# Kernel optimization log

Hardware: AMD Instinct MI355X
Metric: run time of the kernel (lower is better)

## Reference

```python
import jax, jax.numpy as jnp
import numpy as np

B, H, I = 4096, 256, 32


def setup_inputs() -> dict:
    key = jax.random.key(0)
    k1, k2, k3, k4, k5 = jax.random.split(key, 5)
    idx = jax.random.randint(k1, (B,), 0, I)
    inp = jax.nn.one_hot(idx, I, dtype=jnp.float32)  # one-hot selector [B, I]
    hx = jax.random.normal(k2, (B, H), jnp.float32)
    weight_hh = jax.random.normal(k3, (3 * H, H, I), jnp.float32)
    bias_ih = jax.random.normal(k4, (3 * H, I), jnp.float32)
    bias_hh = jax.random.normal(k5, (3 * H, I), jnp.float32)
    return {"input": inp, "hx": hx, "weight_hh": weight_hh,
            "bias_ih": bias_ih, "bias_hh": bias_hh}


def reference(input, hx, weight_hh, bias_ih, bias_hh):
    # input is one-hot, so the broadcast-multiply-sum over the last axis is
    # mathematically a gather of the selected expert slice.
    idx = jnp.argmax(input, axis=-1)                      # [B]
    Wt = jnp.moveaxis(weight_hh, 2, 0)[idx]               # [B, 3H, H] selected recurrent weights
    rec = jnp.einsum('bgh,bh->bg', Wt, hx)                # [B, 3H]
    gates_i = bias_ih.T[idx]                              # [B, 3H]
    gates_h = rec + bias_hh.T[idx]                        # [B, 3H]
    ri, ui, ni = jnp.split(gates_i, 3, axis=1)
    rh, uh, nh = jnp.split(gates_h, 3, axis=1)
    reset_gate = jax.nn.sigmoid(ri + rh)
    update_gate = jax.nn.sigmoid(ui + uh)
    new_gate = jnp.tanh(ni + reset_gate * nh)
    hy = update_gate * hx + (1 - update_gate) * new_gate  # [B, H]
    return hy[None]
```

## Files before the change

kernel.cpp:

```cpp
#include <hip/hip_runtime.h>
#include <math.h>

#define B_N 4096
#define H_N 256
#define I_N 32
#define G3  768

#define NSLOT_AFF 192
#define NSLOT_TOT 336
#define BKT_CAP   24

#define WS_IDX     0
#define WS_SLOTS   16640
#define WS_SORTED  20480
#define WS_B4      36864
#define WS_W5      167936
#define WS_NEEDED  12750848

typedef __attribute__((ext_vector_type(8))) _Float16 f16x8_t;
typedef __attribute__((ext_vector_type(4))) float f32x4_t;

__device__ __forceinline__ float sigm(float x) { return 1.0f / (1.0f + expf(-x)); }

__global__ __launch_bounds__(256) void k_aux(
    const float* __restrict__ w, unsigned short* __restrict__ w5,
    const float* __restrict__ b_ih, const float* __restrict__ b_hh,
    float4* __restrict__ b4,
    const float* __restrict__ inp, int* __restrict__ idx_arr)
{
    int bid = blockIdx.x;
    int t = threadIdx.x;
    if (bid < 768) {
        __shared__ float tl[8 * 1057];
        int r0 = (bid >> 3) * 8;
        int ks = bid & 7;
#pragma unroll
        for (int it = 0; it < 8; ++it) {
            int f4 = it * 256 + t;
            int e4 = (f4 & 7) * 4, hh = (f4 >> 3) & 31, r = f4 >> 8;
            float4 v = *(const float4*)(w + ((size_t)(r0 + r) * 256 + ks * 32 + hh) * 32 + e4);
            int bse = r * 1057 + hh * 33 + e4;
            tl[bse] = v.x; tl[bse + 1] = v.y; tl[bse + 2] = v.z; tl[bse + 3] = v.w;
        }
        __syncthreads();
        int rowgrp = r0 >> 4;
        int mbase = r0 & 15;
#pragma unroll
        for (int it = 0; it < 4; ++it) {
            int c = it * 256 + t;
            int m8 = c & 7, kg = (c >> 3) & 3, e = c >> 5;
            union { _Float16 h[8]; uint4 v; } hi;
#pragma unroll
            for (int t8 = 0; t8 < 8; ++t8) {
                float f = tl[m8 * 1057 + (kg * 8 + t8) * 33 + e];
                hi.h[t8] = (_Float16)f;
            }
            size_t chunk = ((size_t)(e * 8 + ks) * 48 + rowgrp) * 64 + kg * 16 + mbase + m8;
            ((uint4*)w5)[chunk] = hi.v;
        }
    } else if (bid < 800) {
        int bb = bid - 768;
        int e = t & 31;
        int tt = bb * 8 + (t >> 5);
        float r = b_ih[tt * 32 + e] + b_hh[tt * 32 + e];
        float u = b_ih[(256 + tt) * 32 + e] + b_hh[(256 + tt) * 32 + e];
        float ni = b_ih[(512 + tt) * 32 + e];
        float nh = b_hh[(512 + tt) * 32 + e];
        float4 o = {r, u, ni, nh};
        b4[e * 256 + tt] = o;
    } else {
        int b = (bid - 800) * 256 + t;
        const float4* p = (const float4*)(inp + (size_t)b * I_N);
        int idx = 0;
#pragma unroll
        for (int k = 0; k < 8; ++k) {
            float4 v = p[k];
            if (v.x > 0.5f) idx = k * 4 + 0;
            if (v.y > 0.5f) idx = k * 4 + 1;
            if (v.z > 0.5f) idx = k * 4 + 2;
            if (v.w > 0.5f) idx = k * 4 + 3;
        }
        idx_arr[b] = idx;
    }
}

__global__ void k_plan(const int* __restrict__ idx_arr, int* __restrict__ slots,
                       int* __restrict__ sorted) {
    __shared__ int hist[32], offs_l[32], lcur[32];
    __shared__ int bcur[8], ovf;
    int t = threadIdx.x;
    if (t < 32) hist[t] = 0;
    if (t < 8) bcur[t] = 0;
    if (t == 0) ovf = 0;
    __syncthreads();
    for (int i = t; i < B_N; i += 512) atomicAdd(&hist[idx_arr[i]], 1);
    __syncthreads();
    if (t == 0) {
        int run = 0;
        for (int e = 0; e < 32; ++e) { offs_l[e] = run; run += hist[e]; }
    }
    __syncthreads();
    if (t < 32) lcur[t] = offs_l[t];
    for (int s = t; s < NSLOT_TOT; s += 512) slots[s] = -1;
    __syncthreads();
    for (int c = t; c < 32 * 128; c += 512) {
        int e = c >> 7, ch = c & 127;
        int cnt = hist[e];
        if (ch * 32 < cnt) {
            int M = cnt - ch * 32; if (M > 32) M = 32;
            int base = offs_l[e] + ch * 32;
            int item = (e << 18) | (base << 6) | M;
            int bkt = e & 7;
            int j = atomicAdd(&bcur[bkt], 1);
            if (j < BKT_CAP) slots[bkt + 8 * j] = item;
            else { int k = atomicAdd(&ovf, 1); slots[NSLOT_AFF + k] = item; }
        }
    }
    for (int b = t; b < B_N; b += 512) {
        int e = idx_arr[b];
        int pos = atomicAdd(&lcur[e], 1);
        sorted[pos] = b;
    }
}

__global__ __launch_bounds__(256) void k_gemm_mfma(
    const unsigned short* __restrict__ w5,
    const float* __restrict__ hx, const float4* __restrict__ b4,
    const int* __restrict__ sorted, const int* __restrict__ slots,
    float* __restrict__ out)
{
    int item = slots[blockIdx.x];
    if (item < 0) return;
    int e = item >> 18, base = (item >> 6) & 0xfff, M = item & 63;

    __shared__ _Float16 Ah[32 * 256];
    __shared__ int bids[32];

    int t = threadIdx.x;
    {
        int row = t >> 3, c8 = t & 7;
        int b = (row < M) ? sorted[base + row] : -1;
        if (c8 == 0) bids[row] = b;
        if (b >= 0) {
            const float* src = hx + ((size_t)b << 8) + c8 * 32;
            float fv[32];
#pragma unroll
            for (int p = 0; p < 8; ++p)
                *(float4*)&fv[p * 4] = *(const float4*)(src + p * 4);
#pragma unroll
            for (int p = 0; p < 4; ++p) {
                union { _Float16 h[8]; uint4 v; } hu;
#pragma unroll
                for (int jj = 0; jj < 8; ++jj)
                    hu.h[jj] = (_Float16)fv[p * 8 + jj];
                int col = (c8 * 4 + p) ^ (row & 7);
                *(uint4*)&Ah[row * 256 + col * 8] = hu.v;
            }
        } else {
            uint4 z = {0, 0, 0, 0};
#pragma unroll
            for (int p = 0; p < 4; ++p) {
                int col = (c8 * 4 + p) ^ (row & 7);
                *(uint4*)&Ah[row * 256 + col * 8] = z;
            }
        }
    }
    __syncthreads();

    int lane = t & 63, wv = t >> 6;
    int m16 = lane & 15, kg = lane >> 4;
    int q = blockIdx.y * 4 + wv;

    f32x4_t acc[2][3];
#pragma unroll
    for (int tl2 = 0; tl2 < 2; ++tl2)
#pragma unroll
        for (int g = 0; g < 3; ++g) acc[tl2][g] = (f32x4_t){0.f, 0.f, 0.f, 0.f};

    const unsigned short* b_p = w5 + ((size_t)(e * 8) * 48 + q) * 512 + (size_t)lane * 8;

#pragma unroll
    for (int ks = 0; ks < 8; ++ks) {
        int ch = ks * 4 + kg;
        int sw = (ch ^ (m16 & 7)) << 3;
        f16x8_t a_0 = *(const f16x8_t*)&Ah[m16 * 256 + sw];
        f16x8_t a_1 = *(const f16x8_t*)&Ah[(16 + m16) * 256 + sw];
#pragma unroll
        for (int g = 0; g < 3; ++g) {
            size_t foff = ((size_t)ks * 48 + g * 16) * 512;
            f16x8_t b_h = *(const f16x8_t*)(b_p + foff);
            acc[0][g] = __builtin_amdgcn_mfma_f32_16x16x32_f16(a_0, b_h, acc[0][g], 0, 0, 0);
            acc[1][g] = __builtin_amdgcn_mfma_f32_16x16x32_f16(a_1, b_h, acc[1][g], 0, 0, 0);
        }
    }

    int mg = (lane >> 4) * 4;
    int tt = q * 16 + m16;
    float4 bs = b4[e * 256 + tt];
#pragma unroll
    for (int tl2 = 0; tl2 < 2; ++tl2) {
#pragma unroll
        for (int i = 0; i < 4; ++i) {
            int mr = tl2 * 16 + mg + i;
            if (mr < M) {
                int b = bids[mr];
                float x = hx[(size_t)b * 256 + tt];
                float r = sigm(acc[tl2][0][i] + bs.x);
                float u = sigm(acc[tl2][1][i] + bs.y);
                float n = tanhf(bs.z + r * (acc[tl2][2][i] + bs.w));
                out[(size_t)b * 256 + tt] = u * x + (1.0f - u) * n;
            }
        }
    }
}

__global__ void k_naive(const float* __restrict__ inp, const float* __restrict__ hx,
                        const float* __restrict__ w, const float* __restrict__ b_ih,
                        const float* __restrict__ b_hh, float* __restrict__ out) {
    int b = blockIdx.x;
    int t = threadIdx.x;
    __shared__ float sx[H_N];
    __shared__ int sidx;
    if (t == 0) {
        int idx = 0;
        for (int i = 0; i < I_N; ++i)
            if (inp[b * I_N + i] > 0.5f) idx = i;
        sidx = idx;
    }
    sx[t] = hx[b * H_N + t];
    __syncthreads();
    int i = sidx;
    float a0 = 0.f, a1 = 0.f, a2 = 0.f;
    for (int h = 0; h < H_N; ++h) {
        float xv = sx[h];
        a0 = fmaf(w[(t * H_N + h) * I_N + i], xv, a0);
        a1 = fmaf(w[((256 + t) * H_N + h) * I_N + i], xv, a1);
        a2 = fmaf(w[((512 + t) * H_N + h) * I_N + i], xv, a2);
    }
    float r = sigm(b_ih[t * I_N + i] + a0 + b_hh[t * I_N + i]);
    float u = sigm(b_ih[(256 + t) * I_N + i] + a1 + b_hh[(256 + t) * I_N + i]);
    float n = tanhf(b_ih[(512 + t) * I_N + i] + r * (a2 + b_hh[(512 + t) * I_N + i]));
    out[b * H_N + t] = u * sx[t] + (1.0f - u) * n;
}

extern "C" void kernel_launch(void* const* d_in, const int* in_sizes, int n_in,
                              void* d_out, int out_size, void* d_ws, size_t ws_size,
                              hipStream_t stream) {
    const float* inp  = (const float*)d_in[0];
    const float* hx   = (const float*)d_in[1];
    const float* w    = (const float*)d_in[2];
    const float* b_ih = (const float*)d_in[3];
    const float* b_hh = (const float*)d_in[4];
    float* out = (float*)d_out;

    if (ws_size < (size_t)WS_NEEDED) {
        k_naive<<<B_N, H_N, 0, stream>>>(inp, hx, w, b_ih, b_hh, out);
        return;
    }

    char* ws = (char*)d_ws;
    int* idx_arr = (int*)(ws + WS_IDX);
    int* slots   = (int*)(ws + WS_SLOTS);
    int* sorted  = (int*)(ws + WS_SORTED);
    float4* b4   = (float4*)(ws + WS_B4);
    unsigned short* w5 = (unsigned short*)(ws + WS_W5);

    k_aux<<<816, 256, 0, stream>>>(w, w5, b_ih, b_hh, b4, inp, idx_arr);
    k_plan<<<1, 512, 0, stream>>>(idx_arr, slots, sorted);
    k_gemm_mfma<<<dim3(NSLOT_TOT, 4), 256, 0, stream>>>(w5, hx, b4,
                                                        sorted, slots, out);
}
```

Before: 30.26 us.

## Drop single-block planning kernel; bucket rows per segment in aux and plan inside GEMM

Removes the one-block k_plan launch. The index blocks of k_aux now build per-segment expert histograms and local buckets. The GEMM kernel computes per-expert totals and chunk assignments itself and loops over chunks in a grid-stride fashion, finding each row's batch id by prefix-scanning the 16 segment counts. Also switches to __expf-based sigmoid and a fast clamped tanh. This saves one serialized launch and its single-block latency, at the cost of redundant count scans in every GEMM block and slightly lower transcendental accuracy.

```diff
diff --git a/kernel.cpp b/kernel.cpp
--- a/kernel.cpp
+++ b/kernel.cpp
@@ -5,28 +5,31 @@
 #define H_N 256
 #define I_N 32
 #define G3  768
-
-#define NSLOT_AFF 192
-#define NSLOT_TOT 336
-#define BKT_CAP   24
-
-#define WS_IDX     0
-#define WS_SLOTS   16640
-#define WS_SORTED  20480
-#define WS_B4      36864
-#define WS_W5      167936
-#define WS_NEEDED  12750848
+#define NSEG 16
+#define BKROW 4096
+
+#define WS_SC      0
+#define WS_BUCKET  2048
+#define WS_B4      526336
+#define WS_W5      657408
+#define WS_NEEDED  13240320
 
 typedef __attribute__((ext_vector_type(8))) _Float16 f16x8_t;
 typedef __attribute__((ext_vector_type(4))) float f32x4_t;
 
-__device__ __forceinline__ float sigm(float x) { return 1.0f / (1.0f + expf(-x)); }
+__device__ __forceinline__ float sigm(float x) { return 1.0f / (1.0f + __expf(-x)); }
+__device__ __forceinline__ float tanh_fast(float x) {
+    float xc = fminf(fmaxf(x, -15.f), 15.f);
+    float t = __expf(2.f * xc);
+    return (t - 1.f) / (t + 1.f);
+}
 
 __global__ __launch_bounds__(256) void k_aux(
     const float* __restrict__ w, unsigned short* __restrict__ w5,
     const float* __restrict__ b_ih, const float* __restrict__ b_hh,
     float4* __restrict__ b4,
-    const float* __restrict__ inp, int* __restrict__ idx_arr)
+    const float* __restrict__ inp, int* __restrict__ sc,
+    int* __restrict__ bucket)
 {
     int bid = blockIdx.x;
     int t = threadIdx.x;
@@ -69,7 +72,11 @@
         float4 o = {r, u, ni, nh};
         b4[e * 256 + tt] = o;
     } else {
-        int b = (bid - 800) * 256 + t;
+        __shared__ int lhist[32];
+        int seg = bid - 800;
+        if (t < 32) lhist[t] = 0;
+        __syncthreads();
+        int b = seg * 256 + t;
         const float4* p = (const float4*)(inp + (size_t)b * I_N);
         int idx = 0;
 #pragma unroll
@@ -80,67 +87,59 @@
             if (v.z > 0.5f) idx = k * 4 + 2;
             if (v.w > 0.5f) idx = k * 4 + 3;
         }
-        idx_arr[b] = idx;
-    }
-}
-
-__global__ void k_plan(const int* __restrict__ idx_arr, int* __restrict__ slots,
-                       int* __restrict__ sorted) {
-    __shared__ int hist[32], offs_l[32], lcur[32];
-    __shared__ int bcur[8], ovf;
-    int t = threadIdx.x;
-    if (t < 32) hist[t] = 0;
-    if (t < 8) bcur[t] = 0;
-    if (t == 0) ovf = 0;
-    __syncthreads();
-    for (int i = t; i < B_N; i += 512) atomicAdd(&hist[idx_arr[i]], 1);
-    __syncthreads();
-    if (t == 0) {
-        int run = 0;
-        for (int e = 0; e < 32; ++e) { offs_l[e] = run; run += hist[e]; }
-    }
-    __syncthreads();
-    if (t < 32) lcur[t] = offs_l[t];
-    for (int s = t; s < NSLOT_TOT; s += 512) slots[s] = -1;
-    __syncthreads();
-    for (int c = t; c < 32 * 128; c += 512) {
-        int e = c >> 7, ch = c & 127;
-        int cnt = hist[e];
-        if (ch * 32 < cnt) {
-            int M = cnt - ch * 32; if (M > 32) M = 32;
-            int base = offs_l[e] + ch * 32;
-            int item = (e << 18) | (base << 6) | M;
-            int bkt = e & 7;
-            int j = atomicAdd(&bcur[bkt], 1);
-            if (j < BKT_CAP) slots[bkt + 8 * j] = item;
-            else { int k = atomicAdd(&ovf, 1); slots[NSLOT_AFF + k] = item; }
-        }
-    }
-    for (int b = t; b < B_N; b += 512) {
-        int e = idx_arr[b];
-        int pos = atomicAdd(&lcur[e], 1);
-        sorted[pos] = b;
+        int lp = atomicAdd(&lhist[idx], 1);
+        bucket[idx * BKROW + seg * 256 + lp] = b;
+        __syncthreads();
+        if (t < 32) sc[seg * 32 + t] = lhist[t];
     }
 }
 
 __global__ __launch_bounds__(256) void k_gemm_mfma(
     const unsigned short* __restrict__ w5,
     const float* __restrict__ hx, const float4* __restrict__ b4,
-    const int* __restrict__ sorted, const int* __restrict__ slots,
+    const int* __restrict__ sc, const int* __restrict__ bucket,
     float* __restrict__ out)
 {
-    int item = slots[blockIdx.x];
-    if (item < 0) return;
-    int e = item >> 18, base = (item >> 6) & 0xfff, M = item & 63;
+    int bkt = blockIdx.x & 7, j0 = blockIdx.x >> 3;
+    int t = threadIdx.x;
+
+    int tot[4], nch[4];
+#pragma unroll
+    for (int i = 0; i < 4; ++i) {
+        int e = bkt + 8 * i, s = 0;
+#pragma unroll
+        for (int j = 0; j < NSEG; ++j) s += sc[j * 32 + e];
+        tot[i] = s; nch[i] = (s + 31) >> 5;
+    }
+    int c1 = nch[0], c2 = c1 + nch[1], c3 = c2 + nch[2], ntot = c3 + nch[3];
 
     __shared__ _Float16 Ah[32 * 256];
     __shared__ int bids[32];
 
-    int t = threadIdx.x;
-    {
+    for (int jj = j0; jj < ntot; jj += 34) {
+        int ei, ch;
+        if (jj < c1)      { ei = 0; ch = jj; }
+        else if (jj < c2) { ei = 1; ch = jj - c1; }
+        else if (jj < c3) { ei = 2; ch = jj - c2; }
+        else              { ei = 3; ch = jj - c3; }
+        int e = bkt + 8 * ei;
+        int M = tot[ei] - ch * 32; if (M > 32) M = 32;
+
         int row = t >> 3, c8 = t & 7;
-        int b = (row < M) ? sorted[base + row] : -1;
+        int b = -1;
+        if (row < M) {
+            int rank = ch * 32 + row;
+            int acc = 0, seg = 0, off = 0;
+#pragma unroll
+            for (int j = 0; j < NSEG; ++j) {
+                int c = sc[j * 32 + e];
+                if (rank >= acc && rank < acc + c) { seg = j; off = rank - acc; }
+                acc += c;
+            }
+            b = bucket[e * BKROW + seg * 256 + off];
+        }
         if (c8 == 0) bids[row] = b;
+
         if (b >= 0) {
             const float* src = hx + ((size_t)b << 8) + c8 * 32;
             float fv[32];
@@ -151,8 +150,8 @@
             for (int p = 0; p < 4; ++p) {
                 union { _Float16 h[8]; uint4 v; } hu;
 #pragma unroll
-                for (int jj = 0; jj < 8; ++jj)
-                    hu.h[jj] = (_Float16)fv[p * 8 + jj];
+                for (int jj2 = 0; jj2 < 8; ++jj2)
+                    hu.h[jj2] = (_Float16)fv[p * 8 + jj2];
                 int col = (c8 * 4 + p) ^ (row & 7);
                 *(uint4*)&Ah[row * 256 + col * 8] = hu.v;
             }
@@ -164,53 +163,54 @@
                 *(uint4*)&Ah[row * 256 + col * 8] = z;
             }
         }
-    }
-    __syncthreads();
-
-    int lane = t & 63, wv = t >> 6;
-    int m16 = lane & 15, kg = lane >> 4;
-    int q = blockIdx.y * 4 + wv;
-
-    f32x4_t acc[2][3];
-#pragma unroll
-    for (int tl2 = 0; tl2 < 2; ++tl2)
-#pragma unroll
-        for (int g = 0; g < 3; ++g) acc[tl2][g] = (f32x4_t){0.f, 0.f, 0.f, 0.f};
-
-    const unsigned short* b_p = w5 + ((size_t)(e * 8) * 48 + q) * 512 + (size_t)lane * 8;
-
-#pragma unroll
-    for (int ks = 0; ks < 8; ++ks) {
-        int ch = ks * 4 + kg;
-        int sw = (ch ^ (m16 & 7)) << 3;
-        f16x8_t a_0 = *(const f16x8_t*)&Ah[m16 * 256 + sw];
-        f16x8_t a_1 = *(const f16x8_t*)&Ah[(16 + m16) * 256 + sw];
-#pragma unroll
-        for (int g = 0; g < 3; ++g) {
-            size_t foff = ((size_t)ks * 48 + g * 16) * 512;
-            f16x8_t b_h = *(const f16x8_t*)(b_p + foff);
-            acc[0][g] = __builtin_amdgcn_mfma_f32_16x16x32_f16(a_0, b_h, acc[0][g], 0, 0, 0);
-            acc[1][g] = __builtin_amdgcn_mfma_f32_16x16x32_f16(a_1, b_h, acc[1][g], 0, 0, 0);
-        }
-    }
-
-    int mg = (lane >> 4) * 4;
-    int tt = q * 16 + m16;
-    float4 bs = b4[e * 256 + tt];
-#pragma unroll
-    for (int tl2 = 0; tl2 < 2; ++tl2) {
-#pragma unroll
-        for (int i = 0; i < 4; ++i) {
-            int mr = tl2 * 16 + mg + i;
-            if (mr < M) {
-                int b = bids[mr];
-                float x = hx[(size_t)b * 256 + tt];
-                float r = sigm(acc[tl2][0][i] + bs.x);
-                float u = sigm(acc[tl2][1][i] + bs.y);
-                float n = tanhf(bs.z + r * (acc[tl2][2][i] + bs.w));
-                out[(size_t)b * 256 + tt] = u * x + (1.0f - u) * n;
-            }
-        }
+        __syncthreads();
+
+        int lane = t & 63, wv = t >> 6;
+        int m16 = lane & 15, kg = lane >> 4;
+        int q = blockIdx.y * 4 + wv;
+
+        f32x4_t acc2[2][3];
+#pragma unroll
+        for (int tl2 = 0; tl2 < 2; ++tl2)
+#pragma unroll
+            for (int g = 0; g < 3; ++g) acc2[tl2][g] = (f32x4_t){0.f, 0.f, 0.f, 0.f};
+
+        const unsigned short* b_p = w5 + ((size_t)(e * 8) * 48 + q) * 512 + (size_t)lane * 8;
+
+#pragma unroll
+        for (int ks = 0; ks < 8; ++ks) {
+            int chs = ks * 4 + kg;
+            int sw = (chs ^ (m16 & 7)) << 3;
+            f16x8_t a_0 = *(const f16x8_t*)&Ah[m16 * 256 + sw];
+            f16x8_t a_1 = *(const f16x8_t*)&Ah[(16 + m16) * 256 + sw];
+#pragma unroll
+            for (int g = 0; g < 3; ++g) {
+                size_t foff = ((size_t)ks * 48 + g * 16) * 512;
+                f16x8_t b_h = *(const f16x8_t*)(b_p + foff);
+                acc2[0][g] = __builtin_amdgcn_mfma_f32_16x16x32_f16(a_0, b_h, acc2[0][g], 0, 0, 0);
+                acc2[1][g] = __builtin_amdgcn_mfma_f32_16x16x32_f16(a_1, b_h, acc2[1][g], 0, 0, 0);
+            }
+        }
+
+        int mg = (lane >> 4) * 4;
+        int tt = q * 16 + m16;
+        float4 bs = b4[e * 256 + tt];
+#pragma unroll
+        for (int tl2 = 0; tl2 < 2; ++tl2) {
+#pragma unroll
+            for (int i = 0; i < 4; ++i) {
+                int mr = tl2 * 16 + mg + i;
+                if (mr < M) {
+                    int bb = bids[mr];
+                    float x = hx[(size_t)bb * 256 + tt];
+                    float r = sigm(acc2[tl2][0][i] + bs.x);
+                    float u = sigm(acc2[tl2][1][i] + bs.y);
+                    float n = tanh_fast(bs.z + r * (acc2[tl2][2][i] + bs.w));
+                    out[(size_t)bb * 256 + tt] = u * x + (1.0f - u) * n;
+                }
+            }
+        }
+        __syncthreads();
     }
 }
 
@@ -259,14 +259,11 @@
     }
 
     char* ws = (char*)d_ws;
-    int* idx_arr = (int*)(ws + WS_IDX);
-    int* slots   = (int*)(ws + WS_SLOTS);
-    int* sorted  = (int*)(ws + WS_SORTED);
-    float4* b4   = (float4*)(ws + WS_B4);
+    int* sc     = (int*)(ws + WS_SC);
+    int* bucket = (int*)(ws + WS_BUCKET);
+    float4* b4  = (float4*)(ws + WS_B4);
     unsigned short* w5 = (unsigned short*)(ws + WS_W5);
 
-    k_aux<<<816, 256, 0, stream>>>(w, w5, b_ih, b_hh, b4, inp, idx_arr);
-    k_plan<<<1, 512, 0, stream>>>(idx_arr, slots, sorted);
-    k_gemm_mfma<<<dim3(NSLOT_TOT, 4), 256, 0, stream>>>(w5, hx, b4,
-                                                        sorted, slots, out);
-}
+    k_aux<<<816, 256, 0, stream>>>(w, w5, b_ih, b_hh, b4, inp, sc, bucket);
+    k_gemm_mfma<<<dim3(272, 4), 256, 0, stream>>>(w5, hx, b4, sc, bucket, out);
+}
```

New measurement: 28.22 us. -6.8%, faster.
